# Kernel optimization log

Hardware: AMD Instinct MI355X
Metric: run time of the kernel (lower is better)

Reference implementation:

```python
import jax, jax.numpy as jnp
import numpy as np

EPSILON = 1e-8
B, T, H = 4, 4096, 2048          # batch, seq, hidden_dim
D, NH, K = 256, 4, 32            # belief_dim, num_heads, top_k
NB, NG = 65536, 16               # n_beliefs, n_goals
NEG_INF = -1e30


def setup_inputs() -> dict:
    key = jax.random.key(0)
    ks = jax.random.split(key, 8)
    hidden = jax.random.normal(ks[0], (B, T, H), dtype=jnp.float32)
    beliefs = jax.random.normal(ks[1], (NB, D), dtype=jnp.float32)
    active_mask = jax.random.bernoulli(ks[2], 0.5, (NB,))
    goal_embeddings = jax.random.normal(ks[3], (NG, D), dtype=jnp.float32)
    goal_priorities = jax.random.uniform(ks[4], (NG,), dtype=jnp.float32)
    # torch nn.Linear weights are [out_features, in_features]
    Wq = jax.random.normal(ks[5], (NH * D, H), dtype=jnp.float32) / np.float32(np.sqrt(H))
    Wo = jax.random.normal(ks[6], (H, NH * D), dtype=jnp.float32) / np.float32(np.sqrt(NH * D))
    log_temperature = jax.random.normal(ks[7], (NH,), dtype=jnp.float32) * 0.1
    return {"hidden": hidden, "beliefs": beliefs, "active_mask": active_mask,
            "goal_embeddings": goal_embeddings, "goal_priorities": goal_priorities,
            "Wq": Wq, "Wo": Wo, "log_temperature": log_temperature}


def reference(hidden, beliefs, active_mask, goal_embeddings, goal_priorities, Wq, Wo, log_temperature):
    # --- rough-score top-k pre-filter over active beliefs (N_active > top_k path) ---
    mean_query = hidden.mean(axis=(0, 1))                      # [H]
    rough_query = (Wq @ mean_query).reshape(NH, D).mean(axis=0)  # [D]
    radii = jnp.maximum(jnp.linalg.norm(beliefs, axis=-1), EPSILON)  # [NB]
    angles = beliefs / radii[:, None]                          # [NB, D]
    rough_scores = angles @ rough_query                        # [NB]
    # mask-gather: inactive beliefs get -inf so topk selects only active ones
    rough_scores = jnp.where(active_mask, rough_scores, NEG_INF)
    _, topk_idx = jax.lax.top_k(rough_scores, K)               # [K]
    active_beliefs = beliefs[topk_idx]                         # [K, D]

    # --- angle-normalized keys, raw values ---
    a_radii = jnp.maximum(jnp.linalg.norm(active_beliefs, axis=-1), EPSILON)
    keys = active_beliefs / a_radii[:, None]                   # [K, D]
    values = active_beliefs                                    # [K, D]

    # --- per-head queries and temperature ---
    queries = (hidden @ Wq.T).reshape(B, T, NH, D)             # [B,T,h,D]
    temperature = jnp.maximum(jnp.exp(log_temperature), 0.1)   # [h]
    scores = jnp.einsum('bthd,nd->bthn', queries, keys) / np.float32(np.sqrt(D))
    scores = scores * temperature[None, None, :, None]         # [B,T,h,K]

    # --- goal-similarity bias ---
    g_radii = jnp.maximum(jnp.linalg.norm(goal_embeddings, axis=-1), EPSILON)
    goal_angles = goal_embeddings / g_radii[:, None]           # [NG, D]
    sim = (keys @ goal_angles.T) * goal_priorities[None, :]    # [K, NG]
    goal_bias = sim.max(axis=-1)                               # [K], same for all heads
    scores = scores + goal_bias[None, None, None, :]

    attn = jax.nn.softmax(scores, axis=-1)                     # [B,T,h,K]
    retrieved = jnp.einsum('bthn,nd->bthd', attn, values).reshape(B, T, NH * D)
    return retrieved @ Wo.T                                    # [B,T,H]
```

## Files before the change

kernel.cpp:

```cpp
#include <hip/hip_runtime.h>

typedef unsigned int u32;
typedef unsigned short u16;
typedef unsigned long long u64;

typedef __bf16 bf16x8 __attribute__((ext_vector_type(8)));
typedef float f32x4 __attribute__((ext_vector_type(4)));

#define DEV __device__ __forceinline__

DEV u16 f2bf(float f) {
  u32 u = __float_as_uint(f);
  u += 0x7fffu + ((u >> 16) & 1u);
  return (u16)(u >> 16);
}
DEV float bf2f(u16 u) { return __uint_as_float((u32)u << 16); }

DEV void gld_lds16(const void* g, void* l) {
  __builtin_amdgcn_global_load_lds((const __attribute__((address_space(1))) u32*)g,
                                   (__attribute__((address_space(3))) u32*)l, 16, 0, 0);
}

DEV u64 packkey(float f, u32 idx) {
  u32 u = __float_as_uint(f);
  u = (u & 0x80000000u) ? ~u : (u | 0x80000000u);
  return ((u64)u << 32) | (u32)(~idx);
}

__global__ __launch_bounds__(256) void k_conv_mean(const float4* __restrict__ hidden4,
                                                   ushort4* __restrict__ hb4,
                                                   float4* __restrict__ partial4) {
  const int c4 = blockIdx.x * 256 + threadIdx.x;
  const int r0 = blockIdx.y * 64;
  float4 s = {0.f, 0.f, 0.f, 0.f};
  for (int r = 0; r < 64; r++) {
    float4 v = hidden4[(size_t)(r0 + r) * 512 + c4];
    ushort4 o; o.x = f2bf(v.x); o.y = f2bf(v.y); o.z = f2bf(v.z); o.w = f2bf(v.w);
    hb4[(size_t)(r0 + r) * 512 + c4] = o;
    s.x += v.x; s.y += v.y; s.z += v.z; s.w += v.w;
  }
  partial4[blockIdx.y * 512 + c4] = s;
}

__global__ __launch_bounds__(256) void k_mean(const float* __restrict__ partial,
                                              float* __restrict__ mean) {
  __shared__ float red[256];
  const int t = threadIdx.x;
  const int c = t & 15, s = t >> 4;
  const int col = blockIdx.x * 16 + c;
  float acc = 0.f;
  for (int ch = s; ch < 256; ch += 16) acc += partial[ch * 2048 + col];
  red[t] = acc;
  __syncthreads();
  for (int st = 8; st > 0; st >>= 1) {
    if (s < st) red[t] += red[t + st * 16];
    __syncthreads();
  }
  if (s == 0) mean[col] = red[c] * (1.0f / 16384.0f);
}

__global__ __launch_bounds__(256) void k_rq(const float* __restrict__ Wq,
                                            const float* __restrict__ mean,
                                            float* __restrict__ rq) {
  const int w = threadIdx.x >> 6, l = threadIdx.x & 63;
  const int row = blockIdx.x * 4 + w;
  float s = 0.f;
#pragma unroll
  for (int j = 0; j < 32; j++)
    s = fmaf(Wq[(size_t)row * 2048 + j * 64 + l], mean[j * 64 + l], s);
  for (int mk = 1; mk < 64; mk <<= 1) s += __shfl_xor(s, mk);
  if (l == 0) atomicAdd(&rq[row & 255], 0.25f * s);
}

__global__ __launch_bounds__(256) void k_rough(const float* __restrict__ beliefs,
                                               const void* __restrict__ amask,
                                               const float* __restrict__ rq,
                                               u64* __restrict__ keys) {
  const int t = threadIdx.x, w = t >> 6, l = t & 63;
  const int n = blockIdx.x * 4 + w;
  u32 mv = ((const u32*)amask)[l];
  bool isInt = (__ballot(mv > 1u) == 0ull);
  float4 b = *(const float4*)(beliefs + (size_t)n * 256 + l * 4);
  float4 qv = *(const float4*)(rq + l * 4);
  float dot = b.x * qv.x + b.y * qv.y + b.z * qv.z + b.w * qv.w;
  float ss = b.x * b.x + b.y * b.y + b.z * b.z + b.w * b.w;
  for (int mk = 1; mk < 64; mk <<= 1) { dot += __shfl_xor(dot, mk); ss += __shfl_xor(ss, mk); }
  if (l == 0) {
    bool act = isInt ? (((const int*)amask)[n] != 0)
                     : (((const unsigned char*)amask)[n] != 0);
    float score = act ? dot / fmaxf(sqrtf(ss), 1e-8f) : -1e30f;
    keys[n] = packkey(score, (u32)n);
  }
}

__global__ __launch_bounds__(256) void k_topk(const u64* __restrict__ in, int cnt,
                                              u64* __restrict__ outk, int* __restrict__ outi) {
  __shared__ u64 buf[2048];
  __shared__ u64 wmaxS[4];
  const int t = threadIdx.x;
  const int slots = cnt >> 8;
  const u64* src = in + (size_t)blockIdx.x * cnt;
  for (int i = 0; i < slots; i++) buf[t + i * 256] = src[t + i * 256];
  __syncthreads();
  const int l = t & 63, w = t >> 6;
  for (int r = 0; r < 32; r++) {
    u64 m = 0;
    for (int i = 0; i < slots; i++) { u64 v = buf[t + i * 256]; m = v > m ? v : m; }
    for (int mk = 1; mk < 64; mk <<= 1) { u64 o = __shfl_xor(m, mk); m = o > m ? o : m; }
    if (l == 0) wmaxS[w] = m;
    __syncthreads();
    u64 a = wmaxS[0] > wmaxS[1] ? wmaxS[0] : wmaxS[1];
    u64 b = wmaxS[2] > wmaxS[3] ? wmaxS[2] : wmaxS[3];
    u64 win = a > b ? a : b;
    for (int i = 0; i < slots; i++) if (buf[t + i * 256] == win) buf[t + i * 256] = 0ull;
    if (t == 0) {
      if (outk) outk[blockIdx.x * 32 + r] = win;
      if (outi) outi[r] = (int)(~(u32)(win & 0xffffffffull));
    }
    __syncthreads();
  }
}

__global__ __launch_bounds__(256) void k_prep(const float* __restrict__ beliefs,
                                              const float* __restrict__ goals,
                                              const float* __restrict__ prio,
                                              const float* __restrict__ logt,
                                              const int* __restrict__ topk,
                                              float* __restrict__ keysf_g,
                                              float* __restrict__ valsf_g,
                                              float* __restrict__ biasO, float* __restrict__ tempO) {
  __shared__ float keysf[32 * 256];
  __shared__ float gradS[16];
  const int t = threadIdx.x, w = t >> 6, l = t & 63;
  for (int g = w * 4; g < w * 4 + 4; g++) {
    float4 v = *(const float4*)(goals + g * 256 + l * 4);
    float ss = v.x * v.x + v.y * v.y + v.z * v.z + v.w * v.w;
    for (int mk = 1; mk < 64; mk <<= 1) ss += __shfl_xor(ss, mk);
    if (l == 0) gradS[g] = fmaxf(sqrtf(ss), 1e-8f);
  }
  for (int kk = w * 8; kk < w * 8 + 8; kk++) {
    int idx = topk[kk];
    float4 v = *(const float4*)(beliefs + (size_t)idx * 256 + l * 4);
    float ss = v.x * v.x + v.y * v.y + v.z * v.z + v.w * v.w;
    for (int mk = 1; mk < 64; mk <<= 1) ss += __shfl_xor(ss, mk);
    float rr = 1.0f / fmaxf(sqrtf(ss), 1e-8f);
    float4 kv; kv.x = v.x * rr; kv.y = v.y * rr; kv.z = v.z * rr; kv.w = v.w * rr;
    *(float4*)&keysf[kk * 256 + l * 4] = kv;
    *(float4*)&keysf_g[kk * 256 + l * 4] = kv;
    *(float4*)&valsf_g[kk * 256 + l * 4] = v;
  }
  __syncthreads();
  for (int kk = w * 8; kk < w * 8 + 8; kk++) {
    float4 kv = *(const float4*)&keysf[kk * 256 + l * 4];
    float best = -1e30f;
    for (int g = 0; g < 16; g++) {
      float4 gv = *(const float4*)(goals + g * 256 + l * 4);
      float d = kv.x * gv.x + kv.y * gv.y + kv.z * gv.z + kv.w * gv.w;
      for (int mk = 1; mk < 64; mk <<= 1) d += __shfl_xor(d, mk);
      float sim = d / gradS[g] * prio[g];
      best = fmaxf(best, sim);
    }
    if (l == 0) biasO[kk] = best;
  }
  if (t < 4) tempO[t] = fmaxf(__expf(logt[t]), 0.1f);
}

__global__ __launch_bounds__(256) void k_build_kp(const float* __restrict__ Wq,
                                                  const float* __restrict__ keysf_g,
                                                  u16* __restrict__ Kp) {
  __shared__ float keysS[32 * 256];
  __shared__ float WqS[64 * 64];
  const int t = threadIdx.x;
  const int h = blockIdx.x;
  const int c0 = blockIdx.y * 64;
#pragma unroll
  for (int it = 0; it < 32; it++) keysS[t + it * 256] = keysf_g[t + it * 256];
  const int n0 = (t >> 5) * 4;
  const int c2 = (t & 31) * 2;
  float acc[4][2] = {};
  for (int dc = 0; dc < 4; dc++) {
    __syncthreads();
#pragma unroll
    for (int it = 0; it < 16; it++) {
      int i = t + it * 256;
      int r = i >> 6, c = i & 63;
      WqS[i] = Wq[(size_t)(h * 256 + dc * 64 + r) * 2048 + c0 + c];
    }
    __syncthreads();
    for (int d4 = 0; d4 < 16; d4++) {
      float4 kv[4];
#pragma unroll
      for (int i = 0; i < 4; i++)
        kv[i] = *(const float4*)&keysS[(n0 + i) * 256 + dc * 64 + d4 * 4];
#pragma unroll
      for (int dd = 0; dd < 4; dd++) {
        float2 w2 = *(const float2*)&WqS[(d4 * 4 + dd) * 64 + c2];
        float kvd[4] = {kv[0][dd], kv[1][dd], kv[2][dd], kv[3][dd]};
#pragma unroll
        for (int i = 0; i < 4; i++) {
          acc[i][0] = fmaf(kvd[i], w2.x, acc[i][0]);
          acc[i][1] = fmaf(kvd[i], w2.y, acc[i][1]);
        }
      }
    }
  }
#pragma unroll
  for (int i = 0; i < 4; i++) {
    u32 pk = (u32)f2bf(acc[i][0]) | ((u32)f2bf(acc[i][1]) << 16);
    *(u32*)&Kp[(size_t)(h * 32 + n0 + i) * 2048 + c0 + c2] = pk;
  }
}

__global__ __launch_bounds__(256) void k_build_vwo(const float* __restrict__ Wo,
                                                   const float* __restrict__ valsf_g,
                                                   u16* __restrict__ VWoT) {
  __shared__ float valsS[32 * 256];
  __shared__ float WoS[32 * 256];
  const int t = threadIdx.x;
  const int c0 = blockIdx.x * 32;
#pragma unroll
  for (int it = 0; it < 32; it++) valsS[t + it * 256] = valsf_g[t + it * 256];
  const int c = t >> 3;
  const int n0 = (t & 7) * 4;
  for (int h = 0; h < 4; h++) {
    __syncthreads();
#pragma unroll
    for (int it = 0; it < 32; it++) {
      int i = t + it * 256;
      int r = i >> 8, d = i & 255;
      WoS[i] = Wo[(size_t)(c0 + r) * 1024 + h * 256 + d];
    }
    __syncthreads();
    float acc[4] = {};
    for (int d4 = 0; d4 < 64; d4++) {
      float4 w4 = *(const float4*)&WoS[c * 256 + d4 * 4];
#pragma unroll
      for (int i = 0; i < 4; i++) {
        float4 kv = *(const float4*)&valsS[(n0 + i) * 256 + d4 * 4];
        acc[i] = fmaf(w4.x, kv.x, acc[i]);
        acc[i] = fmaf(w4.y, kv.y, acc[i]);
        acc[i] = fmaf(w4.z, kv.z, acc[i]);
        acc[i] = fmaf(w4.w, kv.w, acc[i]);
      }
    }
    ushort4 o; o.x = f2bf(acc[0]); o.y = f2bf(acc[1]); o.z = f2bf(acc[2]); o.w = f2bf(acc[3]);
    *(ushort4*)&VWoT[(size_t)(c0 + c) * 128 + h * 32 + n0] = o;
  }
}

template <typename OutT>
__global__ __launch_bounds__(256) void k_gemm_nt(const u16* __restrict__ A,
                                                 const u16* __restrict__ B,
                                                 OutT* __restrict__ C,
                                                 int N, int lda, int ldb, int kcount, int M) {
  __shared__ __align__(16) u16 As[128 * 32];
  __shared__ __align__(16) u16 Bs[128 * 32];
  const int t = threadIdx.x;
  const int w = t >> 6, l = t & 63;
  const int m0 = blockIdx.y * 128, n0 = blockIdx.x * 128;
  const int p = blockIdx.z;
  const int wm = (w >> 1) * 64, wn = (w & 1) * 64;
  const int c = l & 15, q = l >> 4;
  f32x4 acc[4][4] = {};
  const int rsrc = w * 16 + (l >> 2);
  const int kc = (l & 3) * 8;
  const u16* Ab = A + (size_t)(m0 + rsrc) * lda + (size_t)p * kcount + kc;
  const u16* Bb = B + (size_t)(n0 + rsrc) * ldb + (size_t)p * kcount + kc;
  C += (size_t)p * M * N;
  u16* AsW = &As[w * 512];
  u16* BsW = &Bs[w * 512];
  for (int kt = 0; kt < kcount; kt += 32) {
    gld_lds16(Ab + kt, AsW);
    gld_lds16(Ab + (size_t)64 * lda + kt, AsW + 2048);
    gld_lds16(Bb + kt, BsW);
    gld_lds16(Bb + (size_t)64 * ldb + kt, BsW + 2048);
    __syncthreads();
    bf16x8 af[4], bfr[4];
#pragma unroll
    for (int i = 0; i < 4; i++)
      af[i] = __builtin_bit_cast(bf16x8, *(const uint4*)&As[(wm + i * 16 + c) * 32 + q * 8]);
#pragma unroll
    for (int i = 0; i < 4; i++)
      bfr[i] = __builtin_bit_cast(bf16x8, *(const uint4*)&Bs[(wn + i * 16 + c) * 32 + q * 8]);
#pragma unroll
    for (int mi = 0; mi < 4; mi++)
#pragma unroll
      for (int ni = 0; ni < 4; ni++)
        acc[mi][ni] = __builtin_amdgcn_mfma_f32_16x16x32_bf16(af[mi], bfr[ni], acc[mi][ni], 0, 0, 0);
    __syncthreads();
  }
#pragma unroll
  for (int mi = 0; mi < 4; mi++)
#pragma unroll
    for (int ni = 0; ni < 4; ni++)
#pragma unroll
      for (int r = 0; r < 4; r++) {
        int row = m0 + wm + mi * 16 + q * 4 + r;
        int col = n0 + wn + ni * 16 + c;
        float v = acc[mi][ni][r];
        if constexpr (sizeof(OutT) == 2) C[(size_t)row * N + col] = (OutT)f2bf(v);
        else                             C[(size_t)row * N + col] = v;
      }
}

__global__ __launch_bounds__(256) void k_soft(const u16* __restrict__ Sp,
                                              const float* __restrict__ bias,
                                              const float* __restrict__ temp,
                                              u16* __restrict__ P) {
  __shared__ float biasS[32];
  __shared__ float tS[4];
  const int t = threadIdx.x;
  if (t < 32) biasS[t] = bias[t];
  if (t < 4) tS[t] = temp[t];
  __syncthreads();
  const int w = t >> 6, l = t & 63;
  const int row = blockIdx.x * 4 + w;
  const size_t base = (size_t)row * 128;
  const size_t SPN = (size_t)16384 * 128;
  float s1 = bf2f(Sp[base + l]) + bf2f(Sp[SPN + base + l])
           + bf2f(Sp[2 * SPN + base + l]) + bf2f(Sp[3 * SPN + base + l]);
  float s2 = bf2f(Sp[base + 64 + l]) + bf2f(Sp[SPN + base + 64 + l])
           + bf2f(Sp[2 * SPN + base + 64 + l]) + bf2f(Sp[3 * SPN + base + 64 + l]);
  const int n = l & 31;
  float v1 = fmaf(s1, tS[l >> 5] * 0.0625f, biasS[n]);
  float v2 = fmaf(s2, tS[2 + (l >> 5)] * 0.0625f, biasS[n]);
  float m1 = v1, m2 = v2;
#pragma unroll
  for (int mk = 1; mk <= 16; mk <<= 1) { m1 = fmaxf(m1, __shfl_xor(m1, mk)); m2 = fmaxf(m2, __shfl_xor(m2, mk)); }
  float e1 = __expf(v1 - m1), e2 = __expf(v2 - m2);
  float q1 = e1, q2 = e2;
#pragma unroll
  for (int mk = 1; mk <= 16; mk <<= 1) { q1 += __shfl_xor(q1, mk); q2 += __shfl_xor(q2, mk); }
  P[base + l] = f2bf(e1 / q1);
  P[base + 64 + l] = f2bf(e2 / q2);
}

extern "C" void kernel_launch(void* const* d_in, const int* in_sizes, int n_in,
                              void* d_out, int out_size, void* d_ws, size_t ws_size,
                              hipStream_t stream) {
  const float* hidden = (const float*)d_in[0];
  const float* beliefs = (const float*)d_in[1];
  const void* amask = d_in[2];
  const float* goals = (const float*)d_in[3];
  const float* prio = (const float*)d_in[4];
  const float* Wq = (const float*)d_in[5];
  const float* Wo = (const float*)d_in[6];
  const float* logt = (const float*)d_in[7];
  float* out = (float*)d_out;

  char* ws = (char*)d_ws;
  size_t off = 0;
  auto alloc = [&](size_t bytes) { char* p = ws + off; off = (off + bytes + 255) & ~(size_t)255; return p; };
  u16* hb      = (u16*)alloc(67108864);
  u16* Sp      = (u16*)alloc(16777216);
  u16* P       = (u16*)alloc(4194304);
  u16* kp      = (u16*)alloc(524288);
  u16* vwot    = (u16*)alloc(524288);
  float* partial = (float*)alloc(2097152);
  float* meanq = (float*)alloc(8192);
  float* rq    = (float*)alloc(1024);
  u64* keys    = (u64*)alloc(524288);
  u64* cands   = (u64*)alloc(16384);
  int* topkidx = (int*)alloc(128);
  float* keysf = (float*)alloc(32768);
  float* valsf = (float*)alloc(32768);
  float* biasv = (float*)alloc(128);
  float* tempv = (float*)alloc(16);

  hipMemsetAsync(rq, 0, 1024, stream);
  k_conv_mean<<<dim3(2, 256), 256, 0, stream>>>((const float4*)hidden, (ushort4*)hb, (float4*)partial);
  k_mean<<<128, 256, 0, stream>>>(partial, meanq);
  k_rq<<<256, 256, 0, stream>>>(Wq, meanq, rq);
  k_rough<<<16384, 256, 0, stream>>>(beliefs, amask, rq, keys);
  k_topk<<<64, 256, 0, stream>>>(keys, 1024, cands, nullptr);
  k_topk<<<1, 256, 0, stream>>>(cands, 2048, nullptr, topkidx);
  k_prep<<<1, 256, 0, stream>>>(beliefs, goals, prio, logt, topkidx, keysf, valsf, biasv, tempv);
  k_build_kp<<<dim3(4, 32), 256, 0, stream>>>(Wq, keysf, kp);
  k_build_vwo<<<64, 256, 0, stream>>>(Wo, valsf, vwot);
  k_gemm_nt<u16><<<dim3(1, 128, 4), 256, 0, stream>>>(hb, kp, Sp, 128, 2048, 2048, 512, 16384);
  k_soft<<<4096, 256, 0, stream>>>(Sp, biasv, tempv, P);
  k_gemm_nt<float><<<dim3(16, 128, 1), 256, 0, stream>>>(P, vwot, out, 2048, 128, 128, 128, 16384);
}
```

Measured before the change: 536.9 us.

## Fuse scores GEMM, softmax and output GEMM into one attention kernel

Replaces the split-K score GEMM, the separate softmax kernel and the output GEMM with a single kernel. Each block computes 64 rows of scores against the folded Wq·keys matrix using double-buffered LDS with XOR swizzle, applies softmax in registers, and writes probabilities to LDS. It then multiplies them by the folded V·Wo matrix, streaming output columns. This removes the Sp and P round trips through global memory and several launches. The top-k is also rewritten as register-based wave reductions and fused with prep, and the two weight-folding kernels are merged into one launch. The trade-off is lower parallelism: 256 blocks each do a full K=2048 loop and then write 2048 output columns serially.

```diff
diff --git a/kernel.cpp b/kernel.cpp
--- a/kernel.cpp
+++ b/kernel.cpp
@@ -93,61 +93,94 @@
   }
 }
 
-__global__ __launch_bounds__(256) void k_topk(const u64* __restrict__ in, int cnt,
-                                              u64* __restrict__ outk, int* __restrict__ outi) {
-  __shared__ u64 buf[2048];
-  __shared__ u64 wmaxS[4];
-  const int t = threadIdx.x;
-  const int slots = cnt >> 8;
-  const u64* src = in + (size_t)blockIdx.x * cnt;
-  for (int i = 0; i < slots; i++) buf[t + i * 256] = src[t + i * 256];
-  __syncthreads();
-  const int l = t & 63, w = t >> 6;
+__global__ __launch_bounds__(256) void k_top1(const u64* __restrict__ keys,
+                                              u64* __restrict__ cands) {
+  __shared__ u64 ws[128];
+  const int t = threadIdx.x, w = t >> 6, l = t & 63;
+  const u64* src = keys + (size_t)blockIdx.x * 1024;
+  u64 v0 = src[t], v1 = src[t + 256], v2 = src[t + 512], v3 = src[t + 768];
   for (int r = 0; r < 32; r++) {
-    u64 m = 0;
-    for (int i = 0; i < slots; i++) { u64 v = buf[t + i * 256]; m = v > m ? v : m; }
+    u64 a = v0 > v1 ? v0 : v1;
+    u64 b = v2 > v3 ? v2 : v3;
+    u64 m = a > b ? a : b;
+#pragma unroll
     for (int mk = 1; mk < 64; mk <<= 1) { u64 o = __shfl_xor(m, mk); m = o > m ? o : m; }
-    if (l == 0) wmaxS[w] = m;
-    __syncthreads();
-    u64 a = wmaxS[0] > wmaxS[1] ? wmaxS[0] : wmaxS[1];
-    u64 b = wmaxS[2] > wmaxS[3] ? wmaxS[2] : wmaxS[3];
-    u64 win = a > b ? a : b;
-    for (int i = 0; i < slots; i++) if (buf[t + i * 256] == win) buf[t + i * 256] = 0ull;
-    if (t == 0) {
-      if (outk) outk[blockIdx.x * 32 + r] = win;
-      if (outi) outi[r] = (int)(~(u32)(win & 0xffffffffull));
-    }
-    __syncthreads();
-  }
-}
-
-__global__ __launch_bounds__(256) void k_prep(const float* __restrict__ beliefs,
-                                              const float* __restrict__ goals,
-                                              const float* __restrict__ prio,
-                                              const float* __restrict__ logt,
-                                              const int* __restrict__ topk,
-                                              float* __restrict__ keysf_g,
-                                              float* __restrict__ valsf_g,
-                                              float* __restrict__ biasO, float* __restrict__ tempO) {
+    if (l == 0) ws[w * 32 + r] = m;
+    v0 = (v0 == m) ? 0ull : v0;
+    v1 = (v1 == m) ? 0ull : v1;
+    v2 = (v2 == m) ? 0ull : v2;
+    v3 = (v3 == m) ? 0ull : v3;
+  }
+  __syncthreads();
+  if (w == 0) {
+    u64 u0 = ws[l], u1 = ws[64 + l];
+    for (int r = 0; r < 32; r++) {
+      u64 m = u0 > u1 ? u0 : u1;
+#pragma unroll
+      for (int mk = 1; mk < 64; mk <<= 1) { u64 o = __shfl_xor(m, mk); m = o > m ? o : m; }
+      if (l == 0) cands[blockIdx.x * 32 + r] = m;
+      u0 = (u0 == m) ? 0ull : u0;
+      u1 = (u1 == m) ? 0ull : u1;
+    }
+  }
+}
+
+__global__ __launch_bounds__(256) void k_top2_prep(const u64* __restrict__ cands,
+                                                   const float* __restrict__ beliefs,
+                                                   const float* __restrict__ goals,
+                                                   const float* __restrict__ prio,
+                                                   const float* __restrict__ logt,
+                                                   float* __restrict__ keysf_g,
+                                                   float* __restrict__ valsf_g,
+                                                   float* __restrict__ biasO,
+                                                   float* __restrict__ tempO) {
+  __shared__ u64 ws[128];
+  __shared__ int idxS[32];
   __shared__ float keysf[32 * 256];
   __shared__ float gradS[16];
   const int t = threadIdx.x, w = t >> 6, l = t & 63;
+  u64 v[8];
+#pragma unroll
+  for (int i = 0; i < 8; i++) v[i] = cands[t + i * 256];
+  for (int r = 0; r < 32; r++) {
+    u64 m = v[0];
+#pragma unroll
+    for (int i = 1; i < 8; i++) m = v[i] > m ? v[i] : m;
+#pragma unroll
+    for (int mk = 1; mk < 64; mk <<= 1) { u64 o = __shfl_xor(m, mk); m = o > m ? o : m; }
+    if (l == 0) ws[w * 32 + r] = m;
+#pragma unroll
+    for (int i = 0; i < 8; i++) v[i] = (v[i] == m) ? 0ull : v[i];
+  }
+  __syncthreads();
+  if (w == 0) {
+    u64 u0 = ws[l], u1 = ws[64 + l];
+    for (int r = 0; r < 32; r++) {
+      u64 m = u0 > u1 ? u0 : u1;
+#pragma unroll
+      for (int mk = 1; mk < 64; mk <<= 1) { u64 o = __shfl_xor(m, mk); m = o > m ? o : m; }
+      if (l == 0) idxS[r] = (int)(~(u32)(m & 0xffffffffull));
+      u0 = (u0 == m) ? 0ull : u0;
+      u1 = (u1 == m) ? 0ull : u1;
+    }
+  }
+  __syncthreads();
   for (int g = w * 4; g < w * 4 + 4; g++) {
-    float4 v = *(const float4*)(goals + g * 256 + l * 4);
-    float ss = v.x * v.x + v.y * v.y + v.z * v.z + v.w * v.w;
+    float4 gv = *(const float4*)(goals + g * 256 + l * 4);
+    float ss = gv.x * gv.x + gv.y * gv.y + gv.z * gv.z + gv.w * gv.w;
     for (int mk = 1; mk < 64; mk <<= 1) ss += __shfl_xor(ss, mk);
     if (l == 0) gradS[g] = fmaxf(sqrtf(ss), 1e-8f);
   }
   for (int kk = w * 8; kk < w * 8 + 8; kk++) {
-    int idx = topk[kk];
-    float4 v = *(const float4*)(beliefs + (size_t)idx * 256 + l * 4);
-    float ss = v.x * v.x + v.y * v.y + v.z * v.z + v.w * v.w;
+    int idx = idxS[kk];
+    float4 bv = *(const float4*)(beliefs + (size_t)idx * 256 + l * 4);
+    float ss = bv.x * bv.x + bv.y * bv.y + bv.z * bv.z + bv.w * bv.w;
     for (int mk = 1; mk < 64; mk <<= 1) ss += __shfl_xor(ss, mk);
     float rr = 1.0f / fmaxf(sqrtf(ss), 1e-8f);
-    float4 kv; kv.x = v.x * rr; kv.y = v.y * rr; kv.z = v.z * rr; kv.w = v.w * rr;
+    float4 kv; kv.x = bv.x * rr; kv.y = bv.y * rr; kv.z = bv.z * rr; kv.w = bv.w * rr;
     *(float4*)&keysf[kk * 256 + l * 4] = kv;
     *(float4*)&keysf_g[kk * 256 + l * 4] = kv;
-    *(float4*)&valsf_g[kk * 256 + l * 4] = v;
+    *(float4*)&valsf_g[kk * 256 + l * 4] = bv;
   }
   __syncthreads();
   for (int kk = w * 8; kk < w * 8 + 8; kk++) {
@@ -165,174 +198,229 @@
   if (t < 4) tempO[t] = fmaxf(__expf(logt[t]), 0.1f);
 }
 
-__global__ __launch_bounds__(256) void k_build_kp(const float* __restrict__ Wq,
-                                                  const float* __restrict__ keysf_g,
-                                                  u16* __restrict__ Kp) {
-  __shared__ float keysS[32 * 256];
-  __shared__ float WqS[64 * 64];
+__global__ __launch_bounds__(256) void k_build(const float* __restrict__ Wq,
+                                               const float* __restrict__ Wo,
+                                               const float* __restrict__ keysf_g,
+                                               const float* __restrict__ valsf_g,
+                                               u16* __restrict__ Kp,
+                                               u16* __restrict__ VWoT) {
+  __shared__ __align__(16) float sbuf[16384];
   const int t = threadIdx.x;
-  const int h = blockIdx.x;
-  const int c0 = blockIdx.y * 64;
-#pragma unroll
-  for (int it = 0; it < 32; it++) keysS[t + it * 256] = keysf_g[t + it * 256];
-  const int n0 = (t >> 5) * 4;
-  const int c2 = (t & 31) * 2;
-  float acc[4][2] = {};
-  for (int dc = 0; dc < 4; dc++) {
-    __syncthreads();
-#pragma unroll
-    for (int it = 0; it < 16; it++) {
-      int i = t + it * 256;
-      int r = i >> 6, c = i & 63;
-      WqS[i] = Wq[(size_t)(h * 256 + dc * 64 + r) * 2048 + c0 + c];
-    }
-    __syncthreads();
-    for (int d4 = 0; d4 < 16; d4++) {
-      float4 kv[4];
-#pragma unroll
-      for (int i = 0; i < 4; i++)
-        kv[i] = *(const float4*)&keysS[(n0 + i) * 256 + dc * 64 + d4 * 4];
-#pragma unroll
-      for (int dd = 0; dd < 4; dd++) {
-        float2 w2 = *(const float2*)&WqS[(d4 * 4 + dd) * 64 + c2];
-        float kvd[4] = {kv[0][dd], kv[1][dd], kv[2][dd], kv[3][dd]};
-#pragma unroll
-        for (int i = 0; i < 4; i++) {
-          acc[i][0] = fmaf(kvd[i], w2.x, acc[i][0]);
-          acc[i][1] = fmaf(kvd[i], w2.y, acc[i][1]);
+  if (blockIdx.x < 128) {
+    float* keysS = sbuf;
+    float* WqS = sbuf + 8192;
+    const int h = blockIdx.x >> 5;
+    const int c0 = (blockIdx.x & 31) * 64;
+#pragma unroll
+    for (int it = 0; it < 32; it++) keysS[t + it * 256] = keysf_g[t + it * 256];
+    const int n0 = (t >> 5) * 4;
+    const int c2 = (t & 31) * 2;
+    float acc[4][2] = {};
+    for (int dc = 0; dc < 4; dc++) {
+      __syncthreads();
+#pragma unroll
+      for (int it = 0; it < 16; it++) {
+        int i = t + it * 256;
+        int r = i >> 6, c = i & 63;
+        WqS[i] = Wq[(size_t)(h * 256 + dc * 64 + r) * 2048 + c0 + c];
+      }
+      __syncthreads();
+      for (int d4 = 0; d4 < 16; d4++) {
+        float4 kv[4];
+#pragma unroll
+        for (int i = 0; i < 4; i++)
+          kv[i] = *(const float4*)&keysS[(n0 + i) * 256 + dc * 64 + d4 * 4];
+#pragma unroll
+        for (int dd = 0; dd < 4; dd++) {
+          float2 w2 = *(const float2*)&WqS[(d4 * 4 + dd) * 64 + c2];
+          float kvd[4] = {kv[0][dd], kv[1][dd], kv[2][dd], kv[3][dd]};
+#pragma unroll
+          for (int i = 0; i < 4; i++) {
+            acc[i][0] = fmaf(kvd[i], w2.x, acc[i][0]);
+            acc[i][1] = fmaf(kvd[i], w2.y, acc[i][1]);
+          }
         }
       }
     }
-  }
-#pragma unroll
-  for (int i = 0; i < 4; i++) {
-    u32 pk = (u32)f2bf(acc[i][0]) | ((u32)f2bf(acc[i][1]) << 16);
-    *(u32*)&Kp[(size_t)(h * 32 + n0 + i) * 2048 + c0 + c2] = pk;
-  }
-}
-
-__global__ __launch_bounds__(256) void k_build_vwo(const float* __restrict__ Wo,
-                                                   const float* __restrict__ valsf_g,
-                                                   u16* __restrict__ VWoT) {
-  __shared__ float valsS[32 * 256];
-  __shared__ float WoS[32 * 256];
-  const int t = threadIdx.x;
-  const int c0 = blockIdx.x * 32;
-#pragma unroll
-  for (int it = 0; it < 32; it++) valsS[t + it * 256] = valsf_g[t + it * 256];
-  const int c = t >> 3;
-  const int n0 = (t & 7) * 4;
-  for (int h = 0; h < 4; h++) {
-    __syncthreads();
-#pragma unroll
-    for (int it = 0; it < 32; it++) {
-      int i = t + it * 256;
-      int r = i >> 8, d = i & 255;
-      WoS[i] = Wo[(size_t)(c0 + r) * 1024 + h * 256 + d];
-    }
-    __syncthreads();
-    float acc[4] = {};
-    for (int d4 = 0; d4 < 64; d4++) {
-      float4 w4 = *(const float4*)&WoS[c * 256 + d4 * 4];
-#pragma unroll
-      for (int i = 0; i < 4; i++) {
-        float4 kv = *(const float4*)&valsS[(n0 + i) * 256 + d4 * 4];
-        acc[i] = fmaf(w4.x, kv.x, acc[i]);
-        acc[i] = fmaf(w4.y, kv.y, acc[i]);
-        acc[i] = fmaf(w4.z, kv.z, acc[i]);
-        acc[i] = fmaf(w4.w, kv.w, acc[i]);
+#pragma unroll
+    for (int i = 0; i < 4; i++) {
+      u32 pk = (u32)f2bf(acc[i][0]) | ((u32)f2bf(acc[i][1]) << 16);
+      *(u32*)&Kp[(size_t)(h * 32 + n0 + i) * 2048 + c0 + c2] = pk;
+    }
+  } else {
+    float* valsS = sbuf;
+    float* WoS = sbuf + 8192;
+    const int c0 = (blockIdx.x - 128) * 32;
+#pragma unroll
+    for (int it = 0; it < 32; it++) valsS[t + it * 256] = valsf_g[t + it * 256];
+    const int c = t >> 3;
+    const int n0 = (t & 7) * 4;
+    for (int h = 0; h < 4; h++) {
+      __syncthreads();
+#pragma unroll
+      for (int it = 0; it < 32; it++) {
+        int i = t + it * 256;
+        int r = i >> 8, d = i & 255;
+        WoS[i] = Wo[(size_t)(c0 + r) * 1024 + h * 256 + d];
       }
-    }
-    ushort4 o; o.x = f2bf(acc[0]); o.y = f2bf(acc[1]); o.z = f2bf(acc[2]); o.w = f2bf(acc[3]);
-    *(ushort4*)&VWoT[(size_t)(c0 + c) * 128 + h * 32 + n0] = o;
-  }
-}
-
-template <typename OutT>
-__global__ __launch_bounds__(256) void k_gemm_nt(const u16* __restrict__ A,
-                                                 const u16* __restrict__ B,
-                                                 OutT* __restrict__ C,
-                                                 int N, int lda, int ldb, int kcount, int M) {
-  __shared__ __align__(16) u16 As[128 * 32];
-  __shared__ __align__(16) u16 Bs[128 * 32];
+      __syncthreads();
+      float acc[4] = {};
+      for (int d4 = 0; d4 < 64; d4++) {
+        float4 w4 = *(const float4*)&WoS[c * 256 + d4 * 4];
+#pragma unroll
+        for (int i = 0; i < 4; i++) {
+          float4 kv = *(const float4*)&valsS[(n0 + i) * 256 + d4 * 4];
+          acc[i] = fmaf(w4.x, kv.x, acc[i]);
+          acc[i] = fmaf(w4.y, kv.y, acc[i]);
+          acc[i] = fmaf(w4.z, kv.z, acc[i]);
+          acc[i] = fmaf(w4.w, kv.w, acc[i]);
+        }
+      }
+      ushort4 o; o.x = f2bf(acc[0]); o.y = f2bf(acc[1]); o.z = f2bf(acc[2]); o.w = f2bf(acc[3]);
+      *(ushort4*)&VWoT[(size_t)(c0 + c) * 128 + h * 32 + n0] = o;
+    }
+  }
+}
+
+__global__ __launch_bounds__(512) void k_attn(const u16* __restrict__ hb,
+                                              const u16* __restrict__ kp,
+                                              const u16* __restrict__ vwot,
+                                              const float* __restrict__ bias,
+                                              const float* __restrict__ temp,
+                                              float* __restrict__ out) {
+  __shared__ __align__(16) u16 smem[32768];
+  u16* Plds = smem + 24576;
   const int t = threadIdx.x;
   const int w = t >> 6, l = t & 63;
-  const int m0 = blockIdx.y * 128, n0 = blockIdx.x * 128;
-  const int p = blockIdx.z;
-  const int wm = (w >> 1) * 64, wn = (w & 1) * 64;
-  const int c = l & 15, q = l >> 4;
-  f32x4 acc[4][4] = {};
-  const int rsrc = w * 16 + (l >> 2);
-  const int kc = (l & 3) * 8;
-  const u16* Ab = A + (size_t)(m0 + rsrc) * lda + (size_t)p * kcount + kc;
-  const u16* Bb = B + (size_t)(n0 + rsrc) * ldb + (size_t)p * kcount + kc;
-  C += (size_t)p * M * N;
-  u16* AsW = &As[w * 512];
-  u16* BsW = &Bs[w * 512];
-  for (int kt = 0; kt < kcount; kt += 32) {
-    gld_lds16(Ab + kt, AsW);
-    gld_lds16(Ab + (size_t)64 * lda + kt, AsW + 2048);
-    gld_lds16(Bb + kt, BsW);
-    gld_lds16(Bb + (size_t)64 * ldb + kt, BsW + 2048);
+  const int q = l >> 4, c = l & 15;
+  const int m0 = blockIdx.x * 64;
+  const int rh = w >> 2, hd = w & 3;
+
+  const int rowA = t >> 3;
+  const int cbA = (t & 7) ^ (rowA & 7);
+  const u16* srcA = hb + (size_t)(m0 + rowA) * 2048 + cbA * 8;
+  const int rowB1 = 64 + rowA;
+  const int cbB0 = (t & 7) ^ (rowA & 7);
+  const int cbB1 = (t & 7) ^ (rowB1 & 7);
+  const u16* srcB0 = kp + (size_t)rowA * 2048 + cbB0 * 8;
+  const u16* srcB1 = kp + (size_t)rowB1 * 2048 + cbB1 * 8;
+  u16* dstA = smem + w * 512;
+  u16* dstB0 = smem + 8192 + w * 512;
+  u16* dstB1 = smem + 8192 + 4096 + w * 512;
+
+  f32x4 acc[2][2] = {};
+  gld_lds16(srcA, dstA);
+  gld_lds16(srcB0, dstB0);
+  gld_lds16(srcB1, dstB1);
+  __syncthreads();
+  int buf = 0;
+  for (int s = 0; s < 32; s++) {
+    if (s < 31) {
+      const int kt = (s + 1) * 64;
+      const int bo = buf ^ 1;
+      gld_lds16(srcA + kt, dstA + bo * 4096);
+      gld_lds16(srcB0 + kt, dstB0 + bo * 8192);
+      gld_lds16(srcB1 + kt, dstB1 + bo * 8192);
+    }
+    const u16* Ab = smem + buf * 4096;
+    const u16* Bb = smem + 8192 + buf * 8192;
+    bf16x8 af[2][2], bfr[2][2];
+#pragma unroll
+    for (int mi = 0; mi < 2; mi++) {
+      const int ra = rh * 32 + mi * 16 + c;
+#pragma unroll
+      for (int ks = 0; ks < 2; ks++)
+        af[mi][ks] = __builtin_bit_cast(bf16x8,
+            *(const uint4*)&Ab[ra * 64 + (((ks * 4 + q) ^ (ra & 7)) * 8)]);
+    }
+#pragma unroll
+    for (int ni = 0; ni < 2; ni++) {
+      const int rb = hd * 32 + ni * 16 + c;
+#pragma unroll
+      for (int ks = 0; ks < 2; ks++)
+        bfr[ni][ks] = __builtin_bit_cast(bf16x8,
+            *(const uint4*)&Bb[rb * 64 + (((ks * 4 + q) ^ (rb & 7)) * 8)]);
+    }
+#pragma unroll
+    for (int ks = 0; ks < 2; ks++)
+#pragma unroll
+      for (int mi = 0; mi < 2; mi++)
+#pragma unroll
+        for (int ni = 0; ni < 2; ni++)
+          acc[mi][ni] = __builtin_amdgcn_mfma_f32_16x16x32_bf16(af[mi][ks], bfr[ni][ks],
+                                                                acc[mi][ni], 0, 0, 0);
     __syncthreads();
-    bf16x8 af[4], bfr[4];
-#pragma unroll
-    for (int i = 0; i < 4; i++)
-      af[i] = __builtin_bit_cast(bf16x8, *(const uint4*)&As[(wm + i * 16 + c) * 32 + q * 8]);
-#pragma unroll
-    for (int i = 0; i < 4; i++)
-      bfr[i] = __builtin_bit_cast(bf16x8, *(const uint4*)&Bs[(wn + i * 16 + c) * 32 + q * 8]);
-#pragma unroll
-    for (int mi = 0; mi < 4; mi++)
-#pragma unroll
-      for (int ni = 0; ni < 4; ni++)
-        acc[mi][ni] = __builtin_amdgcn_mfma_f32_16x16x32_bf16(af[mi], bfr[ni], acc[mi][ni], 0, 0, 0);
+    buf ^= 1;
+  }
+
+  const int rowV = t >> 4;
+  const int sltV = t & 15;
+  const int rowV1 = 32 + rowV;
+  const u16* srcV0 = vwot + (size_t)rowV * 128 + ((sltV ^ (rowV & 7)) * 8);
+  const u16* srcV1 = vwot + (size_t)rowV1 * 128 + ((sltV ^ (rowV1 & 7)) * 8);
+  u16* dstV0 = smem + w * 512;
+  u16* dstV1 = smem + 4096 + w * 512;
+  gld_lds16(srcV0, dstV0);
+  gld_lds16(srcV1, dstV1);
+
+  const float ts = temp[hd] * 0.0625f;
+  const float b0 = bias[c], b1 = bias[16 + c];
+#pragma unroll
+  for (int mi = 0; mi < 2; mi++) {
+#pragma unroll
+    for (int r = 0; r < 4; r++) {
+      float v0 = fmaf(acc[mi][0][r], ts, b0);
+      float v1 = fmaf(acc[mi][1][r], ts, b1);
+      float m = fmaxf(v0, v1);
+#pragma unroll
+      for (int mk = 1; mk <= 8; mk <<= 1) m = fmaxf(m, __shfl_xor(m, mk));
+      float e0 = __expf(v0 - m), e1 = __expf(v1 - m);
+      float sum = e0 + e1;
+#pragma unroll
+      for (int mk = 1; mk <= 8; mk <<= 1) sum += __shfl_xor(sum, mk);
+      float inv = 1.0f / sum;
+      const int rp = rh * 32 + mi * 16 + q * 4 + r;
+      const int k0 = hd * 32 + c, k1 = k0 + 16;
+      Plds[rp * 128 + (((k0 >> 3) ^ (rp & 7)) * 8) + (k0 & 7)] = f2bf(e0 * inv);
+      Plds[rp * 128 + (((k1 >> 3) ^ (rp & 7)) * 8) + (k1 & 7)] = f2bf(e1 * inv);
+    }
+  }
+  __syncthreads();
+
+  const int rw = w & 3, chh = w >> 2;
+  int vbuf = 0;
+  for (int cb = 0; cb < 32; cb++) {
+    if (cb < 31) {
+      const size_t so = (size_t)(cb + 1) * 8192;
+      const int bo = vbuf ^ 1;
+      gld_lds16(srcV0 + so, dstV0 + bo * 8192);
+      gld_lds16(srcV1 + so, dstV1 + bo * 8192);
+    }
+    const u16* Vb = smem + vbuf * 8192;
+    f32x4 oacc[2] = {};
+    const int rp = rw * 16 + c;
+#pragma unroll
+    for (int ks = 0; ks < 4; ks++) {
+      bf16x8 pa = __builtin_bit_cast(bf16x8,
+          *(const uint4*)&Plds[rp * 128 + (((ks * 4 + q) ^ (rp & 7)) * 8)]);
+#pragma unroll
+      for (int ni = 0; ni < 2; ni++) {
+        const int rv = chh * 32 + ni * 16 + c;
+        bf16x8 vb = __builtin_bit_cast(bf16x8,
+            *(const uint4*)&Vb[rv * 128 + (((ks * 4 + q) ^ (rv & 7)) * 8)]);
+        oacc[ni] = __builtin_amdgcn_mfma_f32_16x16x32_bf16(pa, vb, oacc[ni], 0, 0, 0);
+      }
+    }
+#pragma unroll
+    for (int ni = 0; ni < 2; ni++) {
+      const int col = cb * 64 + chh * 32 + ni * 16 + c;
+#pragma unroll
+      for (int r = 0; r < 4; r++)
+        out[(size_t)(m0 + rw * 16 + q * 4 + r) * 2048 + col] = oacc[ni][r];
+    }
     __syncthreads();
-  }
-#pragma unroll
-  for (int mi = 0; mi < 4; mi++)
-#pragma unroll
-    for (int ni = 0; ni < 4; ni++)
-#pragma unroll
-      for (int r = 0; r < 4; r++) {
-        int row = m0 + wm + mi * 16 + q * 4 + r;
-        int col = n0 + wn + ni * 16 + c;
-        float v = acc[mi][ni][r];
-        if constexpr (sizeof(OutT) == 2) C[(size_t)row * N + col] = (OutT)f2bf(v);
-        else                             C[(size_t)row * N + col] = v;
-      }
-}
-
-__global__ __launch_bounds__(256) void k_soft(const u16* __restrict__ Sp,
-                                              const float* __restrict__ bias,
-                                              const float* __restrict__ temp,
-                                              u16* __restrict__ P) {
-  __shared__ float biasS[32];
-  __shared__ float tS[4];
-  const int t = threadIdx.x;
-  if (t < 32) biasS[t] = bias[t];
-  if (t < 4) tS[t] = temp[t];
-  __syncthreads();
-  const int w = t >> 6, l = t & 63;
-  const int row = blockIdx.x * 4 + w;
-  const size_t base = (size_t)row * 128;
-  const size_t SPN = (size_t)16384 * 128;
-  float s1 = bf2f(Sp[base + l]) + bf2f(Sp[SPN + base + l])
-           + bf2f(Sp[2 * SPN + base + l]) + bf2f(Sp[3 * SPN + base + l]);
-  float s2 = bf2f(Sp[base + 64 + l]) + bf2f(Sp[SPN + base + 64 + l])
-           + bf2f(Sp[2 * SPN + base + 64 + l]) + bf2f(Sp[3 * SPN + base + 64 + l]);
-  const int n = l & 31;
-  float v1 = fmaf(s1, tS[l >> 5] * 0.0625f, biasS[n]);
-  float v2 = fmaf(s2, tS[2 + (l >> 5)] * 0.0625f, biasS[n]);
-  float m1 = v1, m2 = v2;
-#pragma unroll
-  for (int mk = 1; mk <= 16; mk <<= 1) { m1 = fmaxf(m1, __shfl_xor(m1, mk)); m2 = fmaxf(m2, __shfl_xor(m2, mk)); }
-  float e1 = __expf(v1 - m1), e2 = __expf(v2 - m2);
-  float q1 = e1, q2 = e2;
-#pragma unroll
-  for (int mk = 1; mk <= 16; mk <<= 1) { q1 += __shfl_xor(q1, mk); q2 += __shfl_xor(q2, mk); }
-  P[base + l] = f2bf(e1 / q1);
-  P[base + 64 + l] = f2bf(e2 / q2);
+    vbuf ^= 1;
+  }
 }
 
 extern "C" void kernel_launch(void* const* d_in, const int* in_sizes, int n_in,
@@ -352,8 +440,6 @@
   size_t off = 0;
   auto alloc = [&](size_t bytes) { char* p = ws + off; off = (off + bytes + 255) & ~(size_t)255; return p; };
   u16* hb      = (u16*)alloc(67108864);
-  u16* Sp      = (u16*)alloc(16777216);
-  u16* P       = (u16*)alloc(4194304);
   u16* kp      = (u16*)alloc(524288);
   u16* vwot    = (u16*)alloc(524288);
   float* partial = (float*)alloc(2097152);
@@ -361,7 +447,6 @@
   float* rq    = (float*)alloc(1024);
   u64* keys    = (u64*)alloc(524288);
   u64* cands   = (u64*)alloc(16384);
-  int* topkidx = (int*)alloc(128);
   float* keysf = (float*)alloc(32768);
   float* valsf = (float*)alloc(32768);
   float* biasv = (float*)alloc(128);
@@ -372,12 +457,8 @@
   k_mean<<<128, 256, 0, stream>>>(partial, meanq);
   k_rq<<<256, 256, 0, stream>>>(Wq, meanq, rq);
   k_rough<<<16384, 256, 0, stream>>>(beliefs, amask, rq, keys);
-  k_topk<<<64, 256, 0, stream>>>(keys, 1024, cands, nullptr);
-  k_topk<<<1, 256, 0, stream>>>(cands, 2048, nullptr, topkidx);
-  k_prep<<<1, 256, 0, stream>>>(beliefs, goals, prio, logt, topkidx, keysf, valsf, biasv, tempv);
-  k_build_kp<<<dim3(4, 32), 256, 0, stream>>>(Wq, keysf, kp);
-  k_build_vwo<<<64, 256, 0, stream>>>(Wo, valsf, vwot);
-  k_gemm_nt<u16><<<dim3(1, 128, 4), 256, 0, stream>>>(hb, kp, Sp, 128, 2048, 2048, 512, 16384);
-  k_soft<<<4096, 256, 0, stream>>>(Sp, biasv, tempv, P);
-  k_gemm_nt<float><<<dim3(16, 128, 1), 256, 0, stream>>>(P, vwot, out, 2048, 128, 128, 128, 16384);
-}
+  k_top1<<<64, 256, 0, stream>>>(keys, cands);
+  k_top2_prep<<<1, 256, 0, stream>>>(cands, beliefs, goals, prio, logt, keysf, valsf, biasv, tempv);
+  k_build<<<192, 256, 0, stream>>>(Wq, Wo, keysf, valsf, kp, vwot);
+  k_attn<<<256, 512, 0, stream>>>(hb, kp, vwot, biasv, tempv, out);
+}
```

After: 513.3 us. 4.4% less time.
